# Optimization experiments

Hardware: AMD Instinct MI355X
Metric: run time of the kernel (lower is better)

Reference implementation:

```python
import jax, jax.numpy as jnp
import numpy as np

DIM = 128
HID = 256
NB = 2048      # number of sets (batches)
NTOT = 32768   # total elements across all sets
NMAX = 32      # cap on decoded set size (padded/masked)
VAL_MID = (DIM + HID) // 2    # 192, build_mlp midmult=1.0
SIZE_MID = (HID + 1) // 2     # 128
DEC_MID = (HID + DIM) // 2    # 192


def mish(x):
    return x * jnp.tanh(jax.nn.softplus(x))


def layernorm(x, g, b):
    m = x.mean(-1, keepdims=True)
    v = x.var(-1, keepdims=True)
    return (x - m) / jnp.sqrt(v + 1e-5) * g + b


def _lin_init(key, fan_in, fan_out):
    return jax.random.normal(key, (fan_in, fan_out), jnp.float32) / np.sqrt(fan_in)


def setup_inputs() -> dict:
    key = jax.random.key(0)
    ks = jax.random.split(key, 16)
    x = jax.random.normal(ks[0], (NTOT, DIM), jnp.float32)
    batch = jnp.sort(jax.random.randint(ks[1], (NTOT,), 0, NB)).astype(jnp.int64)
    return {
        "x": x, "batch": batch,
        # encoder rank (Linear(dim,1))
        "rank_w": _lin_init(ks[2], DIM, 1)[:, 0], "rank_b": jnp.zeros((), jnp.float32),
        # encoder val_net: Linear -> LayerNorm -> Mish -> Linear
        "val_w1": _lin_init(ks[3], DIM, VAL_MID), "val_b1": jnp.zeros((VAL_MID,), jnp.float32),
        "val_ln_g": jnp.ones((VAL_MID,), jnp.float32), "val_ln_b": jnp.zeros((VAL_MID,), jnp.float32),
        "val_w2": _lin_init(ks[4], VAL_MID, HID), "val_b2": jnp.zeros((HID,), jnp.float32),
        # shared cardinality Linear(1, hidden)
        "card_w": _lin_init(ks[5], 1, HID), "card_b": jnp.zeros((HID,), jnp.float32),
        # decoder size_pred: Linear -> LayerNorm -> Mish -> Linear
        "size_w1": _lin_init(ks[6], HID, SIZE_MID), "size_b1": jnp.zeros((SIZE_MID,), jnp.float32),
        "size_ln_g": jnp.ones((SIZE_MID,), jnp.float32), "size_ln_b": jnp.zeros((SIZE_MID,), jnp.float32),
        "size_w2": _lin_init(ks[7], SIZE_MID, 1), "size_b2": jnp.zeros((1,), jnp.float32),
        # decoder mlp: Linear -> Mish -> Linear (no layernorm)
        "dec_w1": _lin_init(ks[8], HID, DEC_MID), "dec_b1": jnp.zeros((DEC_MID,), jnp.float32),
        "dec_w2": _lin_init(ks[9], DEC_MID, DIM), "dec_b2": jnp.zeros((DIM,), jnp.float32),
    }


def reference(x, batch, rank_w, rank_b, val_w1, val_b1, val_ln_g, val_ln_b,
              val_w2, val_b2, card_w, card_b, size_w1, size_b1, size_ln_g,
              size_ln_b, size_w2, size_b2, dec_w1, dec_b1, dec_w2, dec_b2):
    batch = batch.astype(jnp.int32)
    t = jnp.linspace(0.0, 1.0, HID)

    # ---- encoder ----
    n = jax.ops.segment_sum(jnp.ones((NTOT,), jnp.float32), batch, num_segments=NB)
    n_i = n.astype(jnp.int32)
    mag = x @ rank_w + rank_b                       # [NTOT]
    # sort within each contiguous batch segment: stable lexsort (batch primary)
    order = jnp.lexsort((mag, batch))
    xs = x[order]
    seg_start = jnp.cumsum(n_i) - n_i               # per-set start offset
    k = (jnp.arange(NTOT, dtype=jnp.int32) - seg_start[batch]).astype(jnp.float32)
    keys = jnp.exp(1j * t[None, :] * k[:, None] * 8.0)            # [NTOT,HID] complex
    h = mish(layernorm(xs @ val_w1 + val_b1, val_ln_g, val_ln_b)) @ val_w2 + val_b2
    y = h.astype(jnp.complex64) * keys
    z_el = jax.ops.segment_sum(y, batch, num_segments=NB)         # [NB,HID] complex
    n_enc = n[:, None] @ card_w + card_b
    z = z_el + n_enc

    # ---- decoder ----
    h2 = mish(layernorm(z.real @ size_w1 + size_b1, size_ln_g, size_ln_b)) @ size_w2 + size_b2
    n_pred = jnp.maximum(jnp.round(h2[:, 0]), 0.0)                # [NB]
    n_pred_i = jnp.minimum(n_pred.astype(jnp.int32), NMAX)
    n_enc2 = n_pred[:, None] @ card_w + card_b
    zc = z - n_enc2
    kk = jnp.arange(NMAX, dtype=jnp.float32)
    keys2 = jnp.exp(1j * t[None, :] * kk[:, None] * 8.0)          # [NMAX,HID]
    zp = zc[:, None, :] * keys2[None, :, :]                       # [NB,NMAX,HID] complex
    xr = mish(zp.real @ dec_w1 + dec_b1) @ dec_w2 + dec_b2        # [NB,NMAX,DIM]
    mask = jnp.arange(NMAX)[None, :] < n_pred_i[:, None]          # [NB,NMAX]
    xr = jnp.where(mask[:, :, None], xr, 0.0)
    return xr, mask, n_pred_i
```

## Files before the change

kernel.cpp:

```cpp
#include <hip/hip_runtime.h>
#include <math.h>

#define DIMX 128
#define HIDX 256
#define NBX 2048
#define NTOTX 32768
#define NMAXX 32
#define VMID 192
#define SMID 128
#define DMID 192

#define EROWS 64
#define SPITCH 66
#define NSEGMAX 128

__device__ __forceinline__ float mishf(float v) {
    if (v > 20.0f) return v;
    float u = expf(v);
    float t = u * (u + 2.0f);
    return v * (t / (t + 2.0f));
}

__global__ __launch_bounds__(512, 4) void k_enc(const float* __restrict__ x,
    const float* __restrict__ rw, const float* __restrict__ rb,
    const float* __restrict__ w1, const float* __restrict__ b1,
    const float* __restrict__ g1, const float* __restrict__ be1,
    const float* __restrict__ w2, const float* __restrict__ b2,
    float* __restrict__ h, float* __restrict__ mag) {
    __shared__ __align__(16) float sbuf[HIDX * SPITCH];
    __shared__ float red[8 * 64];
    __shared__ float red2[8 * 64];
    int tid = threadIdx.x;
    int r = tid & 63;
    int tg = tid >> 6;
    int rowbase = blockIdx.x * EROWS;

#pragma unroll
    for (int it = 0; it < 4; it++) {
        int f4 = it * 512 + tid;
        int rr = f4 >> 5, kq = f4 & 31;
        float4 v = ((const float4*)x)[(size_t)(rowbase + rr) * 32 + kq];
        sbuf[(4 * kq + 0) * SPITCH + rr] = v.x;
        sbuf[(4 * kq + 1) * SPITCH + rr] = v.y;
        sbuf[(4 * kq + 2) * SPITCH + rr] = v.z;
        sbuf[(4 * kq + 3) * SPITCH + rr] = v.w;
    }
    __syncthreads();

    if (tid < 64) {
        float s = 0.0f;
        for (int k = 0; k < DIMX; k++) s += sbuf[k * SPITCH + tid] * rw[k];
        mag[rowbase + tid] = s + rb[0];
    }

    int cb1 = __builtin_amdgcn_readfirstlane(tg * 24);
    float acc[24];
#pragma unroll
    for (int j = 0; j < 24; j++) acc[j] = 0.0f;
#pragma unroll 2
    for (int k = 0; k < DIMX; k++) {
        float xv = sbuf[k * SPITCH + r];
        const float* wr = w1 + k * VMID + cb1;
#pragma unroll
        for (int j = 0; j < 24; j++) acc[j] += wr[j] * xv;
    }

    float part = 0.0f;
#pragma unroll
    for (int j = 0; j < 24; j++) { acc[j] += b1[cb1 + j]; part += acc[j]; }
    red[tg * 64 + r] = part;
    __syncthreads();
    float mean = 0.0f;
#pragma unroll
    for (int q = 0; q < 8; q++) mean += red[q * 64 + r];
    mean *= (1.0f / 192.0f);
    float vpart = 0.0f;
#pragma unroll
    for (int j = 0; j < 24; j++) { acc[j] -= mean; vpart += acc[j] * acc[j]; }
    red2[tg * 64 + r] = vpart;
    __syncthreads();
    float var = 0.0f;
#pragma unroll
    for (int q = 0; q < 8; q++) var += red2[q * 64 + r];
    var *= (1.0f / 192.0f);
    float inv = 1.0f / sqrtf(var + 1e-5f);
#pragma unroll
    for (int j = 0; j < 24; j++)
        acc[j] = mishf(acc[j] * inv * g1[cb1 + j] + be1[cb1 + j]);
#pragma unroll
    for (int j = 0; j < 24; j++) sbuf[(cb1 + j) * SPITCH + r] = acc[j];
    __syncthreads();

    int cb2 = __builtin_amdgcn_readfirstlane(tg * 32);
    float acc2[32];
#pragma unroll
    for (int j = 0; j < 32; j++) acc2[j] = 0.0f;
#pragma unroll 2
    for (int k = 0; k < VMID; k++) {
        float av = sbuf[k * SPITCH + r];
        const float* wr = w2 + k * HIDX + cb2;
#pragma unroll
        for (int j = 0; j < 32; j++) acc2[j] += wr[j] * av;
    }
#pragma unroll
    for (int j = 0; j < 32; j++) acc2[j] += b2[cb2 + j];
    __syncthreads();
#pragma unroll
    for (int j = 0; j < 32; j++) sbuf[(cb2 + j) * SPITCH + r] = acc2[j];
    __syncthreads();

#pragma unroll
    for (int it = 0; it < 8; it++) {
        int f4 = it * 512 + tid;
        int rr = f4 >> 6, cq = f4 & 63;
        float4 v;
        v.x = sbuf[(4 * cq + 0) * SPITCH + rr];
        v.y = sbuf[(4 * cq + 1) * SPITCH + rr];
        v.z = sbuf[(4 * cq + 2) * SPITCH + rr];
        v.w = sbuf[(4 * cq + 3) * SPITCH + rr];
        ((float4*)h)[(size_t)(rowbase + rr) * 64 + cq] = v;
    }
}

__global__ __launch_bounds__(256) void k_z(const float* __restrict__ h,
    const int* __restrict__ batch, const float* __restrict__ mag,
    const float* __restrict__ cw, const float* __restrict__ cb,
    const float* __restrict__ sw1, const float* __restrict__ sb1,
    const float* __restrict__ sg, const float* __restrict__ sbe,
    const float* __restrict__ sw2, const float* __restrict__ sb2,
    float* __restrict__ zcre, float* __restrict__ zim,
    float* __restrict__ out_mask, float* __restrict__ out_np,
    int* __restrict__ npredi) {
    __shared__ float zrow[HIDX];
    __shared__ float magL[NSEGMAX];
    __shared__ int   ordL[NSEGMAX];
    __shared__ int   shs, shn;
    __shared__ float red0[2], red1[2], red2[2];
    int b = blockIdx.x, j = threadIdx.x;
    if (j == 0) {
        int lo = 0, hi = NTOTX;
        while (lo < hi) { int m = (lo + hi) >> 1; if (batch[m] < b) lo = m + 1; else hi = m; }
        int stt = lo;
        hi = NTOTX;
        while (lo < hi) { int m = (lo + hi) >> 1; if (batch[m] <= b) lo = m + 1; else hi = m; }
        shs = stt; shn = lo - stt;
    }
    __syncthreads();
    int s = shs, n_true = shn;
    int n = (n_true < NSEGMAX) ? n_true : NSEGMAX;
    if (j < n) magL[j] = mag[s + j];
    __syncthreads();
    if (j < n) {
        float mi = magL[j];
        int rk = 0;
        for (int q = 0; q < n; q++) {
            float mq = magL[q];
            rk += (mq < mi) || (mq == mi && q < j);
        }
        ordL[rk] = s + j;
    }
    __syncthreads();

    float t = (float)j * (1.0f / 255.0f);
    float zr = 0.f, zi = 0.f;
    int p = 0;
    for (; p + 1 < n; p += 2) {
        int e0 = ordL[p], e1 = ordL[p + 1];
        float hv0 = h[(size_t)e0 * HIDX + j];
        float hv1 = h[(size_t)e1 * HIDX + j];
        float sv0, cv0, sv1, cv1;
        sincosf((t * (float)p) * 8.0f, &sv0, &cv0);
        sincosf((t * (float)(p + 1)) * 8.0f, &sv1, &cv1);
        zr += hv0 * cv0; zi += hv0 * sv0;
        zr += hv1 * cv1; zi += hv1 * sv1;
    }
    if (p < n) {
        int e = ordL[p];
        float hv = h[(size_t)e * HIDX + j];
        float sv, cv;
        sincosf((t * (float)p) * 8.0f, &sv, &cv);
        zr += hv * cv; zi += hv * sv;
    }
    float nf = (float)n_true;
    float zrev = zr + nf * cw[j] + cb[j];
    zrow[j] = zrev;
    zim[(size_t)b * HIDX + j] = zi;
    __syncthreads();

    float v = 0.0f;
    if (j < SMID) {
        v = sb1[j];
        for (int k = 0; k < HIDX; k++) v += zrow[k] * sw1[k * SMID + j];
    }
    float sa = v;
#pragma unroll
    for (int off = 32; off; off >>= 1) sa += __shfl_xor(sa, off, 64);
    if (j < SMID && (j & 63) == 0) red0[j >> 6] = sa;
    __syncthreads();
    float mean = (red0[0] + red0[1]) / 128.0f;
    float d = v - mean;
    float q2 = d * d;
#pragma unroll
    for (int off = 32; off; off >>= 1) q2 += __shfl_xor(q2, off, 64);
    if (j < SMID && (j & 63) == 0) red1[j >> 6] = q2;
    __syncthreads();
    float var = (red1[0] + red1[1]) / 128.0f;
    float p2 = 0.0f;
    if (j < SMID) {
        float lv = d * (1.0f / sqrtf(var + 1e-5f)) * sg[j] + sbe[j];
        p2 = mishf(lv) * sw2[j];
    }
#pragma unroll
    for (int off = 32; off; off >>= 1) p2 += __shfl_xor(p2, off, 64);
    if (j < SMID && (j & 63) == 0) red2[j >> 6] = p2;
    __syncthreads();
    float h2 = red2[0] + red2[1] + sb2[0];
    float npf = fmaxf(rintf(h2), 0.0f);
    int npi = min((int)npf, NMAXX);
    zcre[(size_t)b * HIDX + j] = zrow[j] - (npf * cw[j] + cb[j]);
    if (j < NMAXX) out_mask[b * NMAXX + j] = (j < npi) ? 1.0f : 0.0f;
    if (j == 0) { out_np[b] = (float)npi; npredi[b] = npi; }
}

__global__ __launch_bounds__(256) void k_dec(const float* __restrict__ zcre,
    const float* __restrict__ zim, const int* __restrict__ npredi,
    const float* __restrict__ w1, const float* __restrict__ b1,
    const float* __restrict__ w2, const float* __restrict__ b2,
    float* __restrict__ xr) {
    int m = blockIdx.x, b = blockIdx.y;
    int tid = threadIdx.x;
    size_t row = (size_t)b * NMAXX + m;
    if (m >= npredi[b]) {
        if (tid < DIMX) xr[row * DIMX + tid] = 0.0f;
        return;
    }
    __shared__ float zp[HIDX];
    __shared__ float a[DMID];
    {
        float t = (float)tid * (1.0f / 255.0f);
        float sv, cv;
        sincosf((t * (float)m) * 8.0f, &sv, &cv);
        zp[tid] = zcre[(size_t)b * HIDX + tid] * cv - zim[(size_t)b * HIDX + tid] * sv;
    }
    __syncthreads();
    if (tid < DMID) {
        float v = b1[tid];
#pragma unroll 4
        for (int k = 0; k < HIDX; k++) v += zp[k] * w1[k * DMID + tid];
        a[tid] = mishf(v);
    }
    __syncthreads();
    if (tid < DIMX) {
        float v = b2[tid];
#pragma unroll 4
        for (int k = 0; k < DMID; k++) v += a[k] * w2[k * DIMX + tid];
        xr[row * DIMX + tid] = v;
    }
}

extern "C" void kernel_launch(void* const* d_in, const int* in_sizes, int n_in,
                              void* d_out, int out_size, void* d_ws, size_t ws_size,
                              hipStream_t stream) {
    const float* x      = (const float*)d_in[0];
    const int*   batch  = (const int*)d_in[1];
    const float* rank_w = (const float*)d_in[2];
    const float* rank_b = (const float*)d_in[3];
    const float* vw1    = (const float*)d_in[4];
    const float* vb1    = (const float*)d_in[5];
    const float* vlg    = (const float*)d_in[6];
    const float* vlb    = (const float*)d_in[7];
    const float* vw2    = (const float*)d_in[8];
    const float* vb2    = (const float*)d_in[9];
    const float* cw     = (const float*)d_in[10];
    const float* cb     = (const float*)d_in[11];
    const float* sw1    = (const float*)d_in[12];
    const float* sb1    = (const float*)d_in[13];
    const float* slg    = (const float*)d_in[14];
    const float* slb    = (const float*)d_in[15];
    const float* sw2    = (const float*)d_in[16];
    const float* sb2    = (const float*)d_in[17];
    const float* dw1    = (const float*)d_in[18];
    const float* db1    = (const float*)d_in[19];
    const float* dw2    = (const float*)d_in[20];
    const float* db2    = (const float*)d_in[21];

    char* ws = (char*)d_ws;
    size_t off = 0;
    auto alloc = [&](size_t bytes) {
        void* p = ws + off;
        off += (bytes + 255) & ~(size_t)255;
        return p;
    };
    float* mag  = (float*)alloc((size_t)NTOTX * 4);
    float* zim  = (float*)alloc((size_t)NBX * HIDX * 4);
    float* zcre = (float*)alloc((size_t)NBX * HIDX * 4);
    int*   npi  = (int*)alloc((size_t)NBX * 4);
    float* h    = (float*)alloc((size_t)NTOTX * HIDX * 4);

    float* out_xr   = (float*)d_out;
    float* out_mask = out_xr + (size_t)NBX * NMAXX * DIMX;
    float* out_np   = out_mask + (size_t)NBX * NMAXX;

    hipLaunchKernelGGL(k_enc, dim3(NTOTX / EROWS), dim3(512), 0, stream,
                       x, rank_w, rank_b, vw1, vb1, vlg, vlb, vw2, vb2, h, mag);
    hipLaunchKernelGGL(k_z,   dim3(NBX), dim3(HIDX), 0, stream,
                       h, batch, mag, cw, cb,
                       sw1, sb1, slg, slb, sw2, sb2,
                       zcre, zim, out_mask, out_np, npi);
    hipLaunchKernelGGL(k_dec, dim3(NMAXX, NBX), dim3(256), 0, stream,
                       zcre, zim, npi, dw1, db1, dw2, db2, out_xr);
    (void)in_sizes; (void)n_in; (void)out_size; (void)ws_size;
}
```

Baseline: 145.3 us.

## Split size-prediction MLP into batched kernel and software-pipeline encoder weight loads

The size-prediction MLP moves out of the per-set k_z kernel into a new k_size kernel. Each k_size block handles 8 sets and reuses every sw1 weight load across 4 sets per thread, instead of one block per set with half the threads idle. The encoder GEMM loops now double-buffer weight rows in registers, prefetching the next k rows while the current ones accumulate, and the shared-memory pitch changes from 66 to 65. The split adds a kernel launch and a round trip of z through global memory, and the prefetch buffers raise register pressure under the 512-thread, 4-block launch bounds.

Measured after the change: 257.8 us. 77.4% more time.

```diff
diff --git a/kernel.cpp b/kernel.cpp
--- a/kernel.cpp
+++ b/kernel.cpp
@@ -11,7 +11,7 @@
 #define DMID 192
 
 #define EROWS 64
-#define SPITCH 66
+#define SP 65
 #define NSEGMAX 128
 
 __device__ __forceinline__ float mishf(float v) {
@@ -27,9 +27,9 @@
     const float* __restrict__ g1, const float* __restrict__ be1,
     const float* __restrict__ w2, const float* __restrict__ b2,
     float* __restrict__ h, float* __restrict__ mag) {
-    __shared__ __align__(16) float sbuf[HIDX * SPITCH];
-    __shared__ float red[8 * 64];
-    __shared__ float red2[8 * 64];
+    __shared__ __align__(16) float sbuf[HIDX * SP];
+    __shared__ float red[512];
+    __shared__ float red2[512];
     int tid = threadIdx.x;
     int r = tid & 63;
     int tg = tid >> 6;
@@ -40,29 +40,42 @@
         int f4 = it * 512 + tid;
         int rr = f4 >> 5, kq = f4 & 31;
         float4 v = ((const float4*)x)[(size_t)(rowbase + rr) * 32 + kq];
-        sbuf[(4 * kq + 0) * SPITCH + rr] = v.x;
-        sbuf[(4 * kq + 1) * SPITCH + rr] = v.y;
-        sbuf[(4 * kq + 2) * SPITCH + rr] = v.z;
-        sbuf[(4 * kq + 3) * SPITCH + rr] = v.w;
+        sbuf[(4 * kq + 0) * SP + rr] = v.x;
+        sbuf[(4 * kq + 1) * SP + rr] = v.y;
+        sbuf[(4 * kq + 2) * SP + rr] = v.z;
+        sbuf[(4 * kq + 3) * SP + rr] = v.w;
     }
     __syncthreads();
 
     if (tid < 64) {
         float s = 0.0f;
-        for (int k = 0; k < DIMX; k++) s += sbuf[k * SPITCH + tid] * rw[k];
+        for (int k = 0; k < DIMX; k++) s += sbuf[k * SP + tid] * rw[k];
         mag[rowbase + tid] = s + rb[0];
     }
 
     int cb1 = __builtin_amdgcn_readfirstlane(tg * 24);
+    const float* w1p = w1 + cb1;
     float acc[24];
 #pragma unroll
     for (int j = 0; j < 24; j++) acc[j] = 0.0f;
-#pragma unroll 2
-    for (int k = 0; k < DIMX; k++) {
-        float xv = sbuf[k * SPITCH + r];
-        const float* wr = w1 + k * VMID + cb1;
-#pragma unroll
-        for (int j = 0; j < 24; j++) acc[j] += wr[j] * xv;
+    float wA[24], wB[24];
+#pragma unroll
+    for (int j = 0; j < 24; j++) wA[j] = w1p[j];
+#pragma unroll
+    for (int j = 0; j < 24; j++) wB[j] = w1p[VMID + j];
+    for (int k = 0; k < DIMX; k += 2) {
+        float x0 = sbuf[k * SP + r];
+        float x1 = sbuf[(k + 1) * SP + r];
+        int k2 = (k + 2 < DIMX) ? (k + 2) : k;
+        int k3 = (k + 3 < DIMX) ? (k + 3) : k;
+#pragma unroll
+        for (int j = 0; j < 24; j++) acc[j] += wA[j] * x0;
+#pragma unroll
+        for (int j = 0; j < 24; j++) wA[j] = w1p[k2 * VMID + j];
+#pragma unroll
+        for (int j = 0; j < 24; j++) acc[j] += wB[j] * x1;
+#pragma unroll
+        for (int j = 0; j < 24; j++) wB[j] = w1p[k3 * VMID + j];
     }
 
     float part = 0.0f;
@@ -88,25 +101,38 @@
     for (int j = 0; j < 24; j++)
         acc[j] = mishf(acc[j] * inv * g1[cb1 + j] + be1[cb1 + j]);
 #pragma unroll
-    for (int j = 0; j < 24; j++) sbuf[(cb1 + j) * SPITCH + r] = acc[j];
+    for (int j = 0; j < 24; j++) sbuf[(cb1 + j) * SP + r] = acc[j];
     __syncthreads();
 
     int cb2 = __builtin_amdgcn_readfirstlane(tg * 32);
+    const float* w2p = w2 + cb2;
     float acc2[32];
 #pragma unroll
     for (int j = 0; j < 32; j++) acc2[j] = 0.0f;
-#pragma unroll 2
-    for (int k = 0; k < VMID; k++) {
-        float av = sbuf[k * SPITCH + r];
-        const float* wr = w2 + k * HIDX + cb2;
-#pragma unroll
-        for (int j = 0; j < 32; j++) acc2[j] += wr[j] * av;
+    float vA[32], vB[32];
+#pragma unroll
+    for (int j = 0; j < 32; j++) vA[j] = w2p[j];
+#pragma unroll
+    for (int j = 0; j < 32; j++) vB[j] = w2p[HIDX + j];
+    for (int k = 0; k < VMID; k += 2) {
+        float a0 = sbuf[k * SP + r];
+        float a1 = sbuf[(k + 1) * SP + r];
+        int k2 = (k + 2 < VMID) ? (k + 2) : k;
+        int k3 = (k + 3 < VMID) ? (k + 3) : k;
+#pragma unroll
+        for (int j = 0; j < 32; j++) acc2[j] += vA[j] * a0;
+#pragma unroll
+        for (int j = 0; j < 32; j++) vA[j] = w2p[k2 * HIDX + j];
+#pragma unroll
+        for (int j = 0; j < 32; j++) acc2[j] += vB[j] * a1;
+#pragma unroll
+        for (int j = 0; j < 32; j++) vB[j] = w2p[k3 * HIDX + j];
     }
 #pragma unroll
     for (int j = 0; j < 32; j++) acc2[j] += b2[cb2 + j];
     __syncthreads();
 #pragma unroll
-    for (int j = 0; j < 32; j++) sbuf[(cb2 + j) * SPITCH + r] = acc2[j];
+    for (int j = 0; j < 32; j++) sbuf[(cb2 + j) * SP + r] = acc2[j];
     __syncthreads();
 
 #pragma unroll
@@ -114,10 +140,10 @@
         int f4 = it * 512 + tid;
         int rr = f4 >> 6, cq = f4 & 63;
         float4 v;
-        v.x = sbuf[(4 * cq + 0) * SPITCH + rr];
-        v.y = sbuf[(4 * cq + 1) * SPITCH + rr];
-        v.z = sbuf[(4 * cq + 2) * SPITCH + rr];
-        v.w = sbuf[(4 * cq + 3) * SPITCH + rr];
+        v.x = sbuf[(4 * cq + 0) * SP + rr];
+        v.y = sbuf[(4 * cq + 1) * SP + rr];
+        v.z = sbuf[(4 * cq + 2) * SP + rr];
+        v.w = sbuf[(4 * cq + 3) * SP + rr];
         ((float4*)h)[(size_t)(rowbase + rr) * 64 + cq] = v;
     }
 }
@@ -125,17 +151,10 @@
 __global__ __launch_bounds__(256) void k_z(const float* __restrict__ h,
     const int* __restrict__ batch, const float* __restrict__ mag,
     const float* __restrict__ cw, const float* __restrict__ cb,
-    const float* __restrict__ sw1, const float* __restrict__ sb1,
-    const float* __restrict__ sg, const float* __restrict__ sbe,
-    const float* __restrict__ sw2, const float* __restrict__ sb2,
-    float* __restrict__ zcre, float* __restrict__ zim,
-    float* __restrict__ out_mask, float* __restrict__ out_np,
-    int* __restrict__ npredi) {
-    __shared__ float zrow[HIDX];
+    float* __restrict__ zre, float* __restrict__ zim) {
     __shared__ float magL[NSEGMAX];
     __shared__ int   ordL[NSEGMAX];
     __shared__ int   shs, shn;
-    __shared__ float red0[2], red1[2], red2[2];
     int b = blockIdx.x, j = threadIdx.x;
     if (j == 0) {
         int lo = 0, hi = NTOTX;
@@ -182,44 +201,91 @@
         zr += hv * cv; zi += hv * sv;
     }
     float nf = (float)n_true;
-    float zrev = zr + nf * cw[j] + cb[j];
-    zrow[j] = zrev;
+    zre[(size_t)b * HIDX + j] = zr + nf * cw[j] + cb[j];
     zim[(size_t)b * HIDX + j] = zi;
-    __syncthreads();
-
-    float v = 0.0f;
-    if (j < SMID) {
-        v = sb1[j];
-        for (int k = 0; k < HIDX; k++) v += zrow[k] * sw1[k * SMID + j];
-    }
-    float sa = v;
-#pragma unroll
-    for (int off = 32; off; off >>= 1) sa += __shfl_xor(sa, off, 64);
-    if (j < SMID && (j & 63) == 0) red0[j >> 6] = sa;
-    __syncthreads();
-    float mean = (red0[0] + red0[1]) / 128.0f;
-    float d = v - mean;
-    float q2 = d * d;
-#pragma unroll
-    for (int off = 32; off; off >>= 1) q2 += __shfl_xor(q2, off, 64);
-    if (j < SMID && (j & 63) == 0) red1[j >> 6] = q2;
-    __syncthreads();
-    float var = (red1[0] + red1[1]) / 128.0f;
-    float p2 = 0.0f;
-    if (j < SMID) {
-        float lv = d * (1.0f / sqrtf(var + 1e-5f)) * sg[j] + sbe[j];
-        p2 = mishf(lv) * sw2[j];
-    }
-#pragma unroll
-    for (int off = 32; off; off >>= 1) p2 += __shfl_xor(p2, off, 64);
-    if (j < SMID && (j & 63) == 0) red2[j >> 6] = p2;
-    __syncthreads();
-    float h2 = red2[0] + red2[1] + sb2[0];
-    float npf = fmaxf(rintf(h2), 0.0f);
-    int npi = min((int)npf, NMAXX);
-    zcre[(size_t)b * HIDX + j] = zrow[j] - (npf * cw[j] + cb[j]);
-    if (j < NMAXX) out_mask[b * NMAXX + j] = (j < npi) ? 1.0f : 0.0f;
-    if (j == 0) { out_np[b] = (float)npi; npredi[b] = npi; }
+}
+
+__global__ __launch_bounds__(256) void k_size(const float* __restrict__ zre,
+    const float* __restrict__ cw, const float* __restrict__ cb,
+    const float* __restrict__ sw1, const float* __restrict__ sb1,
+    const float* __restrict__ sg, const float* __restrict__ sbe,
+    const float* __restrict__ sw2, const float* __restrict__ sb2,
+    float* __restrict__ zcre, float* __restrict__ out_mask,
+    float* __restrict__ out_np, int* __restrict__ npredi) {
+    __shared__ float zs[8][HIDX];
+    __shared__ float rA[16], rB[16], rC[16];
+    __shared__ float snpf[8];
+    int tid = threadIdx.x;
+    int b0 = blockIdx.x * 8;
+#pragma unroll
+    for (int it = 0; it < 8; it++) {
+        int idx = it * 256 + tid;
+        zs[idx >> 8][idx & 255] = zre[(size_t)(b0 + (idx >> 8)) * HIDX + (idx & 255)];
+    }
+    __syncthreads();
+
+    int g = tid >> 7;
+    int j = tid & 127;
+    int wv = (tid >> 6) & 1;
+    float acc[4];
+    float vb1 = sb1[j];
+#pragma unroll
+    for (int q = 0; q < 4; q++) acc[q] = vb1;
+    for (int k = 0; k < HIDX; k++) {
+        float w = sw1[k * SMID + j];
+#pragma unroll
+        for (int q = 0; q < 4; q++) acc[q] += zs[g * 4 + q][k] * w;
+    }
+#pragma unroll
+    for (int q = 0; q < 4; q++) {
+        float sa = acc[q];
+#pragma unroll
+        for (int off = 32; off; off >>= 1) sa += __shfl_xor(sa, off, 64);
+        if ((tid & 63) == 0) rA[(g * 2 + wv) * 4 + q] = sa;
+    }
+    __syncthreads();
+    float d[4];
+#pragma unroll
+    for (int q = 0; q < 4; q++) {
+        float mean = (rA[(g * 2) * 4 + q] + rA[(g * 2 + 1) * 4 + q]) / 128.0f;
+        d[q] = acc[q] - mean;
+        float qq = d[q] * d[q];
+#pragma unroll
+        for (int off = 32; off; off >>= 1) qq += __shfl_xor(qq, off, 64);
+        if ((tid & 63) == 0) rB[(g * 2 + wv) * 4 + q] = qq;
+    }
+    __syncthreads();
+    float gj = sg[j], bej = sbe[j], w2j = sw2[j];
+#pragma unroll
+    for (int q = 0; q < 4; q++) {
+        float var = (rB[(g * 2) * 4 + q] + rB[(g * 2 + 1) * 4 + q]) / 128.0f;
+        float lv = d[q] * (1.0f / sqrtf(var + 1e-5f)) * gj + bej;
+        float p2 = mishf(lv) * w2j;
+#pragma unroll
+        for (int off = 32; off; off >>= 1) p2 += __shfl_xor(p2, off, 64);
+        if ((tid & 63) == 0) rC[(g * 2 + wv) * 4 + q] = p2;
+    }
+    __syncthreads();
+    if (tid < 8) {
+        int q = tid & 3, gg = tid >> 2;
+        float h2 = rC[(gg * 2) * 4 + q] + rC[(gg * 2 + 1) * 4 + q] + sb2[0];
+        float npf = fmaxf(rintf(h2), 0.0f);
+        int npi = min((int)npf, NMAXX);
+        snpf[tid] = npf;
+        out_np[b0 + tid] = (float)npi;
+        npredi[b0 + tid] = npi;
+    }
+    __syncthreads();
+#pragma unroll
+    for (int it = 0; it < 8; it++) {
+        int idx = it * 256 + tid;
+        int bi = idx >> 8, jj = idx & 255;
+        zcre[(size_t)(b0 + bi) * HIDX + jj] = zs[bi][jj] - (snpf[bi] * cw[jj] + cb[jj]);
+    }
+    {
+        int bi = tid >> 5, m = tid & 31;
+        out_mask[(b0 + bi) * NMAXX + m] = (m < ((int)fminf(snpf[bi], 32.0f))) ? 1.0f : 0.0f;
+    }
 }
 
 __global__ __launch_bounds__(256) void k_dec(const float* __restrict__ zcre,
@@ -292,6 +358,7 @@
         return p;
     };
     float* mag  = (float*)alloc((size_t)NTOTX * 4);
+    float* zre  = (float*)alloc((size_t)NBX * HIDX * 4);
     float* zim  = (float*)alloc((size_t)NBX * HIDX * 4);
     float* zcre = (float*)alloc((size_t)NBX * HIDX * 4);
     int*   npi  = (int*)alloc((size_t)NBX * 4);
@@ -301,13 +368,14 @@
     float* out_mask = out_xr + (size_t)NBX * NMAXX * DIMX;
     float* out_np   = out_mask + (size_t)NBX * NMAXX;
 
-    hipLaunchKernelGGL(k_enc, dim3(NTOTX / EROWS), dim3(512), 0, stream,
+    hipLaunchKernelGGL(k_enc,  dim3(NTOTX / EROWS), dim3(512), 0, stream,
                        x, rank_w, rank_b, vw1, vb1, vlg, vlb, vw2, vb2, h, mag);
-    hipLaunchKernelGGL(k_z,   dim3(NBX), dim3(HIDX), 0, stream,
-                       h, batch, mag, cw, cb,
-                       sw1, sb1, slg, slb, sw2, sb2,
-                       zcre, zim, out_mask, out_np, npi);
-    hipLaunchKernelGGL(k_dec, dim3(NMAXX, NBX), dim3(256), 0, stream,
+    hipLaunchKernelGGL(k_z,    dim3(NBX), dim3(HIDX), 0, stream,
+                       h, batch, mag, cw, cb, zre, zim);
+    hipLaunchKernelGGL(k_size, dim3(NBX / 8), dim3(256), 0, stream,
+                       zre, cw, cb, sw1, sb1, slg, slb, sw2, sb2,
+                       zcre, out_mask, out_np, npi);
+    hipLaunchKernelGGL(k_dec,  dim3(NMAXX, NBX), dim3(256), 0, stream,
                        zcre, zim, npi, dw1, db1, dw2, db2, out_xr);
     (void)in_sizes; (void)n_in; (void)out_size; (void)ws_size;
 }
```
